# Performance work log

Hardware: AMD Instinct MI355X
Metric: run time of the kernel (lower is better)

Reference implementation:

```python
import jax, jax.numpy as jnp
import numpy as np

# dims (see shape_source)
B, N, P, H, M, E, HOPS = 512, 102, 12, 256, 4, 3, 2
C_CLIP = 10.0   # logit clipping constant params['C']
T = 1.0         # temperature params['T']
NEG = -1e9


def setup_inputs() -> dict:
    key = jax.random.key(0)
    ks = jax.random.split(key, 18)
    s = 0.08  # uniform init range as in _initialize_weights, use scaled normals
    inp = {
        "node_features": jax.random.normal(ks[0], (B, N, P), jnp.float32),
        "adjacency": jax.random.uniform(ks[1], (B, E, N, N), jnp.float32),  # per-edge-cat weighted adjacency
        "mask": jax.random.randint(ks[2], (B, N), 0, 2).astype(jnp.int32),  # 1 = already scheduled / forbidden
        # encoder params
        "W_emb": jax.random.normal(ks[3], (P, H), jnp.float32) * s,
        "W_rel": jax.random.normal(ks[4], (HOPS, E, H, H), jnp.float32) * s / np.sqrt(H),
        "W_self": jax.random.normal(ks[5], (HOPS, H, H), jnp.float32) * s / np.sqrt(H),
        # multi-head glimpse params (Vec / W_q / W_ref per head)
        "Vec": jax.random.normal(ks[6], (M, H, H), jnp.float32) * s,
        "W_q": jax.random.normal(ks[7], (M, 3 * H, H), jnp.float32) * s,
        "W_ref": jax.random.normal(ks[8], (M, H, H), jnp.float32) * s,
        "W_mh": jax.random.normal(ks[9], (M * H, H), jnp.float32) * s,  # multi_head_embedding
        # final pointer params
        "Vec2": jax.random.normal(ks[10], (H,), jnp.float32) * s,
        "W_q2": jax.random.normal(ks[11], (H, H), jnp.float32) * s,
        "W_ref2": jax.random.normal(ks[12], (H, H), jnp.float32) * s,
        # learned decoder seed vectors
        "dec_input": jax.random.normal(ks[13], (H,), jnp.float32) * s,
        "v_1": jax.random.normal(ks[14], (H,), jnp.float32) * s,
    }
    return inp


def reference(node_features, adjacency, mask, W_emb, W_rel, W_self, Vec, W_q,
              W_ref, W_mh, Vec2, W_q2, W_ref2, dec_input, v_1):
    # ---- encoder: linear embedding + HOPS of relational (per-edge-category) message passing ----
    h = jnp.einsum('bnp,ph->bnh', node_features, W_emb)            # [B,N,H]
    for hop in range(HOPS):
        msg = jnp.einsum('benm,bmh->benh', adjacency, h)           # gather neighbors per edge cat
        h = jax.nn.relu(jnp.einsum('benh,ehk->bnk', msg, W_rel[hop])
                        + jnp.einsum('bnh,hk->bnk', h, W_self[hop]))
    enc = h                                                         # [B,N,H]

    # ---- decoder query: cat(graph readout, learned dec_input, learned v_1) -> 3H ----
    enc_mean = enc.mean(axis=1)                                     # [B,H]
    q_cat = jnp.concatenate([enc_mean,
                             jnp.broadcast_to(dec_input, (B, H)),
                             jnp.broadcast_to(v_1, (B, H))], axis=-1)  # [B,3H]

    # ---- multi-head additive (Bahdanau) glimpse: per-head Vec/W_q/W_ref tanh scoring ----
    q = jnp.einsum('bf,mfh->bmh', q_cat, W_q)                       # [B,M,H]
    r = jnp.einsum('bnh,mhk->bmnk', enc, W_ref)                     # [B,M,N,H]
    u = jnp.einsum('bmnh,mhk->bmnk', jnp.tanh(q[:, :, None, :] + r), Vec)
    scores = u.sum(axis=-1)                                         # [B,M,N]
    scores = jnp.where(mask[:, None, :] > 0, NEG, scores)
    a = jax.nn.softmax(scores, axis=-1)
    ctx = jnp.einsum('bmn,bnh->bmh', a, enc).reshape(B, M * H)
    query2 = ctx @ W_mh                                             # [B,H]

    # ---- final pointer head (Vec2 / W_q2 / W_ref2) ----
    u2 = jnp.einsum('h,bnh->bn', Vec2,
                    jnp.tanh((query2 @ W_q2)[:, None, :] + jnp.einsum('bnh,hk->bnk', enc, W_ref2)))
    u2 = C_CLIP * jnp.tanh(u2)                                      # logit clipping
    u2 = jnp.where(mask > 0, NEG, u2)
    log_p = jax.nn.log_softmax(u2 / T, axis=-1)                     # [B,N]
    return log_p
```

## Files before the change

### kernel.cpp

```cpp
#include <hip/hip_runtime.h>
#include <hip/hip_bf16.h>

#define B 512
#define N 102
#define Pdim 12
#define H 256
#define M 4
#define E 3
#define NEG (-1e9f)
#define RT 52224
#define NN 10404

typedef __hip_bfloat16 bf16;
typedef __attribute__((ext_vector_type(8))) short short8;
typedef __attribute__((ext_vector_type(4))) float f32x4;
typedef __attribute__((ext_vector_type(16))) float f32x16;

__device__ __forceinline__ float b2f(bf16 v) { return __bfloat162float(v); }
__device__ __forceinline__ bf16 f2b(float v) { return __float2bfloat16(v); }
__device__ __forceinline__ short f2bs(float v) {
    bf16 t = __float2bfloat16(v);
    return *reinterpret_cast<short*>(&t);
}
__device__ __forceinline__ float fast_tanh(float x) {
    float e = __expf(2.f * x);
    return 1.f - 2.f * __builtin_amdgcn_rcpf(e + 1.f);
}

__global__ __launch_bounds__(256) void wt_prep(const float* __restrict__ Wrel,
                                               const float* __restrict__ Wself,
                                               const float* __restrict__ Wref,
                                               const float* __restrict__ Wref2,
                                               const float* __restrict__ Wmh,
                                               const float* __restrict__ Wq2,
                                               const float* __restrict__ W_q,
                                               const float* __restrict__ Vec,
                                               const float* __restrict__ W_emb,
                                               const float* __restrict__ dec,
                                               const float* __restrict__ v1,
                                               short* __restrict__ wfrag,
                                               short* __restrict__ wrefT,
                                               short* __restrict__ wref2T,
                                               short* __restrict__ wmh_bf,
                                               short* __restrict__ wq2_bf,
                                               short* __restrict__ wq_bf,
                                               short* __restrict__ wembf,
                                               float* __restrict__ qconst,
                                               float* __restrict__ vsum) {
    int bid = blockIdx.x;
    int tid = threadIdx.x;
    __shared__ short tl[1024 * 17];
    if (bid < 32) {
        int hop = bid >> 4, ct = bid & 15;
        for (int i = tid; i < 16384; i += 256) {
            int k = i >> 4, c0 = i & 15;
            int c = ct * 16 + c0;
            float v;
            if (k < 768) v = Wrel[(((size_t)hop * E + (k >> 8)) * H + (k & 255)) * H + c];
            else         v = Wself[((size_t)hop * H + (k - 768)) * H + c];
            tl[k * 17 + c0] = f2bs(v);
        }
        __syncthreads();
        short8* outp = (short8*)wfrag + (size_t)(hop * 16 + ct) * 2048;
        for (int i = tid; i < 2048; i += 256) {
            int ks = i >> 6, lq = i & 63;
            int c0 = lq & 15, kb = (lq >> 4) * 8;
            short8 v;
#pragma unroll
            for (int j = 0; j < 8; ++j) v[j] = tl[(ks * 32 + kb + j) * 17 + c0];
            outp[i] = v;
        }
        return;
    }
    if (bid >= 3648) {
        int m = bid - 3648, hh = tid;
        __shared__ float dls[H], vls[H];
        dls[hh] = dec[hh];
        vls[hh] = v1[hh];
        __syncthreads();
        const float* Wm = W_q + (size_t)m * (3 * H) * H;
        float s = 0.f;
        for (int f = 0; f < H; ++f)
            s += dls[f] * Wm[(H + f) * H + hh] + vls[f] * Wm[(2 * H + f) * H + hh];
        qconst[m * H + hh] = s;
        float vs = 0.f;
        const float* Vr = Vec + ((size_t)m * H + hh) * H;
        for (int k = 0; k < H; ++k) vs += Vr[k];
        vsum[m * H + hh] = vs;
        return;
    }
    int idx = 524288 + (bid - 32) * 256 + tid;
    if (idx < 786432) {
        int r = idx - 524288;
        int row = r >> 8, k = r & 255;
        int m = row >> 8, c = row & 255;
        wrefT[r] = f2bs(Wref[((size_t)m * H + k) * H + c]);
    } else if (idx < 851968) {
        int r = idx - 786432;
        int c = r >> 8, k = r & 255;
        wref2T[r] = f2bs(Wref2[k * H + c]);
    } else if (idx < 1114112) {
        int r = idx - 851968;
        wmh_bf[r] = f2bs(Wmh[r]);
    } else if (idx < 1179648) {
        int r = idx - 1114112;
        wq2_bf[r] = f2bs(Wq2[r]);
    } else if (idx < 1441792) {
        int r = idx - 1179648;
        int m = r >> 16, fh = r & 65535;
        wq_bf[r] = f2bs(W_q[(size_t)m * 768 * 256 + fh]);
    } else if (idx < 1449984) {
        int r = idx - 1441792;
        int ct = r >> 9, lq = (r >> 3) & 63, j = r & 7;
        int c = ct * 16 + (lq & 15), k = (lq >> 4) * 8 + j;
        wembf[r] = (k < Pdim) ? f2bs(W_emb[k * H + c]) : (short)0;
    }
}

#define HP 264
#define YTP 136
#define ASP 136
#define AITER 21
__global__ __launch_bounds__(512, 2) void hop_fused(const bf16* __restrict__ hin,
                                                    const float* __restrict__ nf,
                                                    const short* __restrict__ wembf,
                                                    const float* __restrict__ adj,
                                                    const short* __restrict__ wfragp,
                                                    bf16* __restrict__ hout,
                                                    float* __restrict__ mean_out) {
    int b = blockIdx.x;
    int tid = threadIdx.x;
    int w = tid >> 6;
    int l = tid & 63;
    int cg = l & 15;
    int rg = l >> 4;
    int ct0 = 2 * w, ct1 = 2 * w + 1;

    __shared__ short hS[112 * HP];
    __shared__ short YtS[8 * 32 * YTP];
    __shared__ short AsS[112 * ASP];

    const short8 z8 = {0, 0, 0, 0, 0, 0, 0, 0};
    for (int i = tid; i < (8 * 32 * YTP) / 8; i += 512) ((short8*)YtS)[i] = z8;
    for (int i = tid; i < 10 * 32; i += 512) {
        int n = 102 + (i >> 5), g = i & 31;
        *(short8*)(&hS[n * HP + g * 8]) = z8;
    }
    for (int i = tid; i < 112 * 26; i += 512) {
        int n = i / 26, m = 102 + (i % 26);
        AsS[n * ASP + m] = 0;
    }
    for (int i = tid; i < 10 * 102; i += 512) {
        int n = 102 + i / 102, m = i % 102;
        AsS[n * ASP + m] = 0;
    }
    int offA[AITER];
    {
        const float* Ab0 = adj + (size_t)b * E * NN;
#pragma unroll
        for (int i = 0; i < AITER; ++i) {
            int id = tid + (i << 9);
            if (id < NN) {
                int n = id / N, m = id - n * N;
                offA[i] = n * ASP + m;
                AsS[offA[i]] = f2bs(Ab0[id]);
            } else offA[i] = -1;
        }
    }
    float areg[AITER];
    {
        const float* Ab1 = adj + ((size_t)b * E + 1) * NN;
#pragma unroll
        for (int i = 0; i < AITER; ++i) {
            int id = tid + (i << 9);
            areg[i] = (id < NN) ? Ab1[id] : 0.f;
        }
    }
    if (hin) {
        const short* hp = (const short*)hin;
        for (int i = tid; i < 102 * 32; i += 512) {
            int n = i >> 5, g = i & 31;
            *(short8*)(&hS[n * HP + g * 8]) = *(const short8*)(hp + ((size_t)b * N + n) * H + g * 8);
        }
    } else {
        const short8* we8 = (const short8*)wembf;
        short8 bf0 = we8[ct0 * 64 + l];
        short8 bf1 = we8[ct1 * 64 + l];
#pragma unroll
        for (int nt = 0; nt < 7; ++nt) {
            int row = nt * 16 + cg;
            short8 afr = z8;
            if (row < 102 && rg < 2) {
                const float* src = nf + ((size_t)b * N + row) * Pdim + rg * 8;
                f32x4 v0 = *(const f32x4*)src;
                afr[0] = f2bs(v0[0]); afr[1] = f2bs(v0[1]);
                afr[2] = f2bs(v0[2]); afr[3] = f2bs(v0[3]);
                if (rg == 0) {
                    f32x4 v1 = *(const f32x4*)(src + 4);
                    afr[4] = f2bs(v1[0]); afr[5] = f2bs(v1[1]);
                    afr[6] = f2bs(v1[2]); afr[7] = f2bs(v1[3]);
                }
            }
            f32x4 d0 = (f32x4){0.f, 0.f, 0.f, 0.f}, d1 = d0;
            d0 = __builtin_amdgcn_mfma_f32_16x16x32_bf16(afr, bf0, d0, 0, 0, 0);
            d1 = __builtin_amdgcn_mfma_f32_16x16x32_bf16(afr, bf1, d1, 0, 0, 0);
#pragma unroll
            for (int r = 0; r < 4; ++r) {
                int n = nt * 16 + rg * 4 + r;
                hS[n * HP + ct0 * 16 + cg] = f2bs(d0[r]);
                hS[n * HP + ct1 * 16 + cg] = f2bs(d1[r]);
            }
        }
    }
    __syncthreads();

    const short8* wf8 = (const short8*)wfragp;
    f32x4 hacc0[7], hacc1[7];
#pragma unroll
    for (int j = 0; j < 7; ++j) {
        hacc0[j] = (f32x4){0.f, 0.f, 0.f, 0.f};
        hacc1[j] = hacc0[j];
    }

#pragma unroll
    for (int ks = 0; ks < 8; ++ks) {
        short8 wfs0 = wf8[(ct0 * 32 + 24 + ks) * 64 + l];
        short8 wfs1 = wf8[(ct1 * 32 + 24 + ks) * 64 + l];
#pragma unroll
        for (int nt = 0; nt < 7; ++nt) {
            short8 hf = *(const short8*)(&hS[(nt * 16 + cg) * HP + ks * 32 + rg * 8]);
            hacc0[nt] = __builtin_amdgcn_mfma_f32_16x16x32_bf16(hf, wfs0, hacc0[nt], 0, 0, 0);
            hacc1[nt] = __builtin_amdgcn_mfma_f32_16x16x32_bf16(hf, wfs1, hacc1[nt], 0, 0, 0);
        }
    }

    int ytbase = w * (32 * YTP);
    for (int e = 0; e < E; ++e) {
        if (e > 0) {
            __syncthreads();
#pragma unroll
            for (int i = 0; i < AITER; ++i)
                if (offA[i] >= 0) AsS[offA[i]] = f2bs(areg[i]);
            if (e < E - 1) {
                const float* Abn = adj + ((size_t)b * E + e + 1) * NN;
#pragma unroll
                for (int i = 0; i < AITER; ++i) {
                    int id = tid + (i << 9);
                    if (id < NN) areg[i] = Abn[id];
                }
            }
            __syncthreads();
        }
        f32x4 g0[7], g1[7];
#pragma unroll
        for (int j = 0; j < 7; ++j) {
            g0[j] = (f32x4){0.f, 0.f, 0.f, 0.f};
            g1[j] = g0[j];
        }
#pragma unroll
        for (int ks = 0; ks < 8; ++ks) {
            short8 wfa0 = wf8[(ct0 * 32 + e * 8 + ks) * 64 + l];
            short8 wfa1 = wf8[(ct1 * 32 + e * 8 + ks) * 64 + l];
#pragma unroll
            for (int mt = 0; mt < 7; ++mt) {
                short8 hf = *(const short8*)(&hS[(mt * 16 + cg) * HP + ks * 32 + rg * 8]);
                g0[mt] = __builtin_amdgcn_mfma_f32_16x16x32_bf16(wfa0, hf, g0[mt], 0, 0, 0);
                g1[mt] = __builtin_amdgcn_mfma_f32_16x16x32_bf16(wfa1, hf, g1[mt], 0, 0, 0);
            }
        }
#pragma unroll
        for (int mt = 0; mt < 7; ++mt) {
            int gl = mt * 2 + (cg >> 3);
            int gp0 = ((gl + rg) & 15) * 8 + (cg & 7);
            int gp1 = ((gl + 4 + rg) & 15) * 8 + (cg & 7);
#pragma unroll
            for (int r = 0; r < 4; ++r) {
                YtS[ytbase + (rg * 4 + r) * YTP + gp0] = f2bs(g0[mt][r]);
                YtS[ytbase + (16 + rg * 4 + r) * YTP + gp1] = f2bs(g1[mt][r]);
            }
        }
#pragma unroll
        for (int ks = 0; ks < 4; ++ks) {
            short8 yf0 = *(const short8*)(&YtS[ytbase + cg * YTP +
                                               (((ks * 4 + rg) + (cg >> 2)) & 15) * 8]);
            short8 yf1 = *(const short8*)(&YtS[ytbase + (16 + cg) * YTP +
                                               (((ks * 4 + rg) + 4 + (cg >> 2)) & 15) * 8]);
#pragma unroll
            for (int nt = 0; nt < 7; ++nt) {
                short8 af = *(const short8*)(&AsS[(nt * 16 + cg) * ASP + ks * 32 + rg * 8]);
                hacc0[nt] = __builtin_amdgcn_mfma_f32_16x16x32_bf16(af, yf0, hacc0[nt], 0, 0, 0);
                hacc1[nt] = __builtin_amdgcn_mfma_f32_16x16x32_bf16(af, yf1, hacc1[nt], 0, 0, 0);
            }
        }
    }
    __syncthreads();
#pragma unroll
    for (int nt = 0; nt < 7; ++nt)
#pragma unroll
        for (int r = 0; r < 4; ++r) {
            int n = nt * 16 + rg * 4 + r;
            float v0 = hacc0[nt][r], v1 = hacc1[nt][r];
            hS[n * HP + ct0 * 16 + cg] = f2bs(v0 > 0.f ? v0 : 0.f);
            hS[n * HP + ct1 * 16 + cg] = f2bs(v1 > 0.f ? v1 : 0.f);
        }
    __syncthreads();
    short* ho = (short*)hout;
    for (int i = tid; i < 102 * 32; i += 512) {
        int n = i >> 5, g = i & 31;
        *(short8*)(ho + ((size_t)b * N + n) * H + g * 8) = *(const short8*)(&hS[n * HP + g * 8]);
    }
    if (mean_out) {
        float* partf = (float*)AsS;
        int c = tid & 255, qq = tid >> 8;
        float s = 0.f;
        for (int n = qq; n < N; n += 2) s += b2f(*(const bf16*)&hS[n * HP + c]);
        partf[qq * 256 + c] = s;
        __syncthreads();
        if (tid < 256)
            mean_out[(size_t)b * H + tid] =
                (partf[tid] + partf[256 + tid]) * (1.f / (float)N);
    }
}

__global__ __launch_bounds__(256, 2) void head2_mfma(const bf16* __restrict__ X,
                                                     const short* __restrict__ WT,
                                                     const float* __restrict__ qb, int qbs,
                                                     const float* __restrict__ vsb,
                                                     float* __restrict__ outp, int obs) {
    int rt = blockIdx.x, m = blockIdx.y;
    int r0 = rt * 128;
    int tid = threadIdx.x;
    int w = tid >> 6, l = tid & 63;
    int lr = l & 31;
    int lh = l >> 5;
    __shared__ short Xs[128 * 256];
    __shared__ float qls[3 * 256];
    __shared__ float part[4][128];

    const short* Xp = (const short*)X;
#pragma unroll
    for (int i = 0; i < 16; ++i) {
        int id = tid + i * 256;
        int r = id >> 5, g = id & 31;
        short8 v = *(const short8*)(Xp + (size_t)(r0 + r) * H + g * 8);
        *(short8*)((char*)Xs + r * 512 + ((g ^ (r & 7)) * 16)) = v;
    }
    int b_base = r0 / N;
#pragma unroll
    for (int i = 0; i < 3; ++i) {
        int bb = b_base + i;
        if (bb > B - 1) bb = B - 1;
        qls[i * 256 + tid] = qb[(size_t)bb * qbs + m * H + tid];
    }
    const short8* w8 = (const short8*)WT;
    int cbase = m * 256 + w * 64;
    short8 afr0[16], afr1[16];
#pragma unroll
    for (int ks = 0; ks < 16; ++ks) {
        afr0[ks] = w8[(size_t)(cbase + lr) * 32 + ks * 2 + lh];
        afr1[ks] = w8[(size_t)(cbase + 32 + lr) * 32 + ks * 2 + lh];
    }
    float vsl[32];
#pragma unroll
    for (int j = 0; j < 16; ++j) {
        int cl = (j & 3) + 8 * (j >> 2) + 4 * lh;
        vsl[j]      = vsb[m * H + w * 64 + cl];
        vsl[16 + j] = vsb[m * H + w * 64 + 32 + cl];
    }
    __syncthreads();

    int swz = lr & 7;
    for (int t = 0; t < 4; ++t) {
        f32x16 acc0, acc1;
#pragma unroll
        for (int j = 0; j < 16; ++j) { acc0[j] = 0.f; acc1[j] = 0.f; }
        const char* xbase = (const char*)Xs + (t * 32 + lr) * 512;
#pragma unroll
        for (int ks = 0; ks < 16; ++ks) {
            short8 bx = *(const short8*)(xbase + (((2 * ks + lh) ^ swz) * 16));
            acc0 = __builtin_amdgcn_mfma_f32_32x32x16_bf16(afr0[ks], bx, acc0, 0, 0, 0);
            acc1 = __builtin_amdgcn_mfma_f32_32x32x16_bf16(afr1[ks], bx, acc1, 0, 0, 0);
        }
        int r = r0 + t * 32 + lr;
        int b = r / N;
        int boff = b - b_base;
        float s = 0.f;
#pragma unroll
        for (int j = 0; j < 16; ++j) {
            int cl = (j & 3) + 8 * (j >> 2) + 4 * lh;
            float x0 = qls[boff * 256 + w * 64 + cl] + acc0[j];
            s += fast_tanh(x0) * vsl[j];
            float x1 = qls[boff * 256 + w * 64 + 32 + cl] + acc1[j];
            s += fast_tanh(x1) * vsl[16 + j];
        }
        s += __shfl_xor(s, 32, 64);
        if (l < 32) part[w][t * 32 + lr] = s;
    }
    __syncthreads();
    if (tid < 128) {
        int r = r0 + tid;
        int b = r / N, n = r - b * N;
        outp[(size_t)b * obs + m * N + n] = part[0][tid] + part[1][tid] + part[2][tid] + part[3][tid];
    }
}

__global__ __launch_bounds__(256) void q_k(const float* __restrict__ enc_mean,
                                           const short* __restrict__ wq_bf,
                                           const float* __restrict__ qconst,
                                           float* __restrict__ qbuf) {
    int bid = blockIdx.x;
    int b = bid >> 2, m = bid & 3;
    int hh = threadIdx.x;
    __shared__ float em[H];
    em[hh] = enc_mean[(size_t)b * H + hh];
    __syncthreads();
    const bf16* Wm = (const bf16*)(wq_bf + (size_t)m * 65536);
    float s = qconst[m * H + hh];
    for (int f = 0; f < H; ++f) s += em[f] * b2f(Wm[f * H + hh]);
    qbuf[((size_t)b * M + m) * H + hh] = s;
}

__global__ __launch_bounds__(256) void softmax_ctx_k(const float* __restrict__ scores,
                                                     const int* __restrict__ mask,
                                                     const bf16* __restrict__ enc,
                                                     float* __restrict__ ctx) {
    int bid = blockIdx.x;
    int b = bid >> 2, m = bid & 3;
    int tid = threadIdx.x;
    __shared__ float a[128];
    __shared__ float red[2];
    float sv = NEG;
    if (tid < N)
        sv = (mask[(size_t)b * N + tid] > 0) ? NEG : scores[((size_t)b * M + m) * N + tid];
    if (tid < 128) a[tid] = sv;
    __syncthreads();
    if (tid < 64) {
        float v = fmaxf(a[tid], a[tid + 64]);
        v = fmaxf(v, __shfl_xor(v, 32, 64));
        v = fmaxf(v, __shfl_xor(v, 16, 64));
        v = fmaxf(v, __shfl_xor(v, 8, 64));
        v = fmaxf(v, __shfl_xor(v, 4, 64));
        v = fmaxf(v, __shfl_xor(v, 2, 64));
        v = fmaxf(v, __shfl_xor(v, 1, 64));
        if (tid == 0) red[0] = v;
    }
    __syncthreads();
    float mx = red[0];
    float ev = (tid < N) ? __expf(sv - mx) : 0.f;
    if (tid < 128) a[tid] = ev;
    __syncthreads();
    if (tid < 64) {
        float v = a[tid] + a[tid + 64];
        v += __shfl_xor(v, 32, 64);
        v += __shfl_xor(v, 16, 64);
        v += __shfl_xor(v, 8, 64);
        v += __shfl_xor(v, 4, 64);
        v += __shfl_xor(v, 2, 64);
        v += __shfl_xor(v, 1, 64);
        if (tid == 0) red[1] = __builtin_amdgcn_rcpf(v);
    }
    __syncthreads();
    float inv = red[1];
    float c = 0.f;
    for (int n = 0; n < N; ++n)
        c += a[n] * b2f(enc[((size_t)b * N + n) * H + tid]);
    ctx[((size_t)b * M + m) * H + tid] = c * inv;
}

__global__ __launch_bounds__(256) void query2_k(const float* __restrict__ ctx,
                                                const short* __restrict__ wmh,
                                                const short* __restrict__ wq2,
                                                float* __restrict__ q2) {
    int b = blockIdx.x;
    int tid = threadIdx.x;
    __shared__ float cx[M * H];
    __shared__ float qy[H];
    for (int idx = tid; idx < M * H; idx += 256) cx[idx] = ctx[(size_t)b * M * H + idx];
    __syncthreads();
    const bf16* wm = (const bf16*)wmh;
    float acc = 0.f;
    for (int j = 0; j < M * H; ++j) acc += cx[j] * b2f(wm[(size_t)j * H + tid]);
    qy[tid] = acc;
    __syncthreads();
    const bf16* w2 = (const bf16*)wq2;
    float acc2 = 0.f;
    for (int k = 0; k < H; ++k) acc2 += qy[k] * b2f(w2[(size_t)k * H + tid]);
    q2[(size_t)b * H + tid] = acc2;
}

__global__ __launch_bounds__(128) void final_out_k(const float* __restrict__ u2,
                                                   const int* __restrict__ mask,
                                                   float* __restrict__ out) {
    int b = blockIdx.x;
    int tid = threadIdx.x;
    __shared__ float a[128];
    __shared__ float red[2];
    float u = NEG;
    if (tid < N) {
        u = 10.f * fast_tanh(u2[(size_t)b * N + tid]);
        if (mask[(size_t)b * N + tid] > 0) u = NEG;
    }
    a[tid] = u;
    __syncthreads();
    if (tid < 64) {
        float v = fmaxf(a[tid], a[tid + 64]);
        v = fmaxf(v, __shfl_xor(v, 32, 64));
        v = fmaxf(v, __shfl_xor(v, 16, 64));
        v = fmaxf(v, __shfl_xor(v, 8, 64));
        v = fmaxf(v, __shfl_xor(v, 4, 64));
        v = fmaxf(v, __shfl_xor(v, 2, 64));
        v = fmaxf(v, __shfl_xor(v, 1, 64));
        if (tid == 0) red[0] = v;
    }
    __syncthreads();
    float mx = red[0];
    float ev = (tid < N) ? __expf(u - mx) : 0.f;
    a[tid] = ev;
    __syncthreads();
    if (tid < 64) {
        float v = a[tid] + a[tid + 64];
        v += __shfl_xor(v, 32, 64);
        v += __shfl_xor(v, 16, 64);
        v += __shfl_xor(v, 8, 64);
        v += __shfl_xor(v, 4, 64);
        v += __shfl_xor(v, 2, 64);
        v += __shfl_xor(v, 1, 64);
        if (tid == 0) red[1] = logf(v);
    }
    __syncthreads();
    if (tid < N) out[(size_t)b * N + tid] = (u - mx) - red[1];
}

extern "C" void kernel_launch(void* const* d_in, const int* in_sizes, int n_in,
                              void* d_out, int out_size, void* d_ws, size_t ws_size,
                              hipStream_t stream) {
    const float* nf     = (const float*)d_in[0];
    const float* adj    = (const float*)d_in[1];
    const int*   mask   = (const int*)d_in[2];
    const float* W_emb  = (const float*)d_in[3];
    const float* W_rel  = (const float*)d_in[4];
    const float* W_self = (const float*)d_in[5];
    const float* Vec    = (const float*)d_in[6];
    const float* W_q    = (const float*)d_in[7];
    const float* W_ref  = (const float*)d_in[8];
    const float* W_mh   = (const float*)d_in[9];
    const float* Vec2   = (const float*)d_in[10];
    const float* W_q2   = (const float*)d_in[11];
    const float* W_ref2 = (const float*)d_in[12];
    const float* dec    = (const float*)d_in[13];
    const float* v_1    = (const float*)d_in[14];
    float* out = (float*)d_out;

    char* p = (char*)d_ws;
    size_t off = 0;
    auto alloc = [&](size_t bytes) -> char* {
        char* q = p + off;
        off += (bytes + 255) & ~(size_t)255;
        return q;
    };
    bf16* hA    = (bf16*)alloc((size_t)RT * H * sizeof(bf16));
    bf16* hB    = (bf16*)alloc((size_t)RT * H * sizeof(bf16));
    short* wfrag  = (short*)alloc(524288 * sizeof(short));
    short* wrefT  = (short*)alloc(262144 * sizeof(short));
    short* wref2T = (short*)alloc(65536 * sizeof(short));
    short* wmh_bf = (short*)alloc(262144 * sizeof(short));
    short* wq2_bf = (short*)alloc(65536 * sizeof(short));
    short* wq_bf  = (short*)alloc(262144 * sizeof(short));
    short* wembf  = (short*)alloc(8192 * sizeof(short));
    float* enc_mean = (float*)alloc((size_t)B * H * sizeof(float));
    float* qconst   = (float*)alloc((size_t)M * H * sizeof(float));
    float* vsumb    = (float*)alloc((size_t)M * H * sizeof(float));
    float* qbuf     = (float*)alloc((size_t)B * M * H * sizeof(float));
    float* scoresb  = (float*)alloc((size_t)B * M * N * sizeof(float));
    float* ctxb     = (float*)alloc((size_t)B * M * H * sizeof(float));
    float* q2b      = (float*)alloc((size_t)B * H * sizeof(float));
    float* u2b      = (float*)alloc((size_t)B * N * sizeof(float));

    wt_prep<<<3652, 256, 0, stream>>>(W_rel, W_self, W_ref, W_ref2, W_mh, W_q2,
                                      W_q, Vec, W_emb, dec, v_1,
                                      wfrag, wrefT, wref2T, wmh_bf, wq2_bf, wq_bf, wembf,
                                      qconst, vsumb);

    hop_fused<<<B, 512, 0, stream>>>(nullptr, nf, wembf, adj, wfrag, hB, nullptr);
    hop_fused<<<B, 512, 0, stream>>>(hB, nullptr, wembf, adj, wfrag + 262144, hA, enc_mean);

    const bf16* enc = hA;

    q_k<<<B * M, 256, 0, stream>>>(enc_mean, wq_bf, qconst, qbuf);
    head2_mfma<<<dim3(RT / 128, M), 256, 0, stream>>>(enc, wrefT, qbuf, M * H, vsumb, scoresb, M * N);
    softmax_ctx_k<<<B * M, 256, 0, stream>>>(scoresb, mask, enc, ctxb);
    query2_k<<<B, 256, 0, stream>>>(ctxb, wmh_bf, wq2_bf, q2b);
    head2_mfma<<<dim3(RT / 128, 1), 256, 0, stream>>>(enc, wref2T, q2b, H, Vec2, u2b, N);
    final_out_k<<<B, 128, 0, stream>>>(u2b, mask, out);
}
```

Measured before the change: 331.4 us.

## Fuse both encoder hops into one kernel with pre-padded bf16 adjacency

```diff
diff --git a/kernel.cpp b/kernel.cpp
--- a/kernel.cpp
+++ b/kernel.cpp
@@ -38,6 +38,7 @@
                                                const float* __restrict__ W_emb,
                                                const float* __restrict__ dec,
                                                const float* __restrict__ v1,
+                                               const float* __restrict__ adj,
                                                short* __restrict__ wfrag,
                                                short* __restrict__ wrefT,
                                                short* __restrict__ wref2T,
@@ -45,11 +46,24 @@
                                                short* __restrict__ wq2_bf,
                                                short* __restrict__ wq_bf,
                                                short* __restrict__ wembf,
+                                               short* __restrict__ adjp,
                                                float* __restrict__ qconst,
                                                float* __restrict__ vsum) {
     int bid = blockIdx.x;
     int tid = threadIdx.x;
     __shared__ short tl[1024 * 17];
+    if (bid >= 3652) {
+        int be = bid - 3652;
+        const float* src = adj + (size_t)be * NN;
+        short* dst = adjp + (size_t)be * (112 * 128);
+        for (int i = tid; i < 112 * 128; i += 256) {
+            int n = i >> 7, m = i & 127;
+            short v = 0;
+            if (n < N && m < N) v = f2bs(src[n * N + m]);
+            dst[i] = v;
+        }
+        return;
+    }
     if (bid < 32) {
         int hop = bid >> 4, ct = bid & 15;
         for (int i = tid; i < 16384; i += 256) {
@@ -118,15 +132,13 @@
 }
 
 #define HP 264
-#define YTP 136
+#define YP2 136
 #define ASP 136
-#define AITER 21
-__global__ __launch_bounds__(512, 2) void hop_fused(const bf16* __restrict__ hin,
-                                                    const float* __restrict__ nf,
+__global__ __launch_bounds__(512, 2) void enc_fused(const float* __restrict__ nf,
                                                     const short* __restrict__ wembf,
-                                                    const float* __restrict__ adj,
+                                                    const short* __restrict__ adjp,
                                                     const short* __restrict__ wfragp,
-                                                    bf16* __restrict__ hout,
+                                                    bf16* __restrict__ enc_out,
                                                     float* __restrict__ mean_out) {
     int b = blockIdx.x;
     int tid = threadIdx.x;
@@ -134,58 +146,26 @@
     int l = tid & 63;
     int cg = l & 15;
     int rg = l >> 4;
-    int ct0 = 2 * w, ct1 = 2 * w + 1;
+    int ct0 = 2 * w, ct1 = ct0 + 1;
 
     __shared__ short hS[112 * HP];
-    __shared__ short YtS[8 * 32 * YTP];
+    __shared__ short YtS[256 * YP2];
     __shared__ short AsS[112 * ASP];
 
     const short8 z8 = {0, 0, 0, 0, 0, 0, 0, 0};
-    for (int i = tid; i < (8 * 32 * YTP) / 8; i += 512) ((short8*)YtS)[i] = z8;
     for (int i = tid; i < 10 * 32; i += 512) {
         int n = 102 + (i >> 5), g = i & 31;
         *(short8*)(&hS[n * HP + g * 8]) = z8;
     }
-    for (int i = tid; i < 112 * 26; i += 512) {
-        int n = i / 26, m = 102 + (i % 26);
-        AsS[n * ASP + m] = 0;
-    }
-    for (int i = tid; i < 10 * 102; i += 512) {
-        int n = 102 + i / 102, m = i % 102;
-        AsS[n * ASP + m] = 0;
-    }
-    int offA[AITER];
     {
-        const float* Ab0 = adj + (size_t)b * E * NN;
-#pragma unroll
-        for (int i = 0; i < AITER; ++i) {
-            int id = tid + (i << 9);
-            if (id < NN) {
-                int n = id / N, m = id - n * N;
-                offA[i] = n * ASP + m;
-                AsS[offA[i]] = f2bs(Ab0[id]);
-            } else offA[i] = -1;
-        }
-    }
-    float areg[AITER];
+        int c = tid >> 1, g = 14 + (tid & 1);
+        *(short8*)(&YtS[c * YP2 + g * 8]) = z8;
+    }
+
     {
-        const float* Ab1 = adj + ((size_t)b * E + 1) * NN;
-#pragma unroll
-        for (int i = 0; i < AITER; ++i) {
-            int id = tid + (i << 9);
-            areg[i] = (id < NN) ? Ab1[id] : 0.f;
-        }
-    }
-    if (hin) {
-        const short* hp = (const short*)hin;
-        for (int i = tid; i < 102 * 32; i += 512) {
-            int n = i >> 5, g = i & 31;
-            *(short8*)(&hS[n * HP + g * 8]) = *(const short8*)(hp + ((size_t)b * N + n) * H + g * 8);
-        }
-    } else {
         const short8* we8 = (const short8*)wembf;
-        short8 bf0 = we8[ct0 * 64 + l];
-        short8 bf1 = we8[ct1 * 64 + l];
+        short8 bfe0 = we8[ct0 * 64 + l];
+        short8 bfe1 = we8[ct1 * 64 + l];
 #pragma unroll
         for (int nt = 0; nt < 7; ++nt) {
             int row = nt * 16 + cg;
@@ -202,8 +182,8 @@
                 }
             }
             f32x4 d0 = (f32x4){0.f, 0.f, 0.f, 0.f}, d1 = d0;
-            d0 = __builtin_amdgcn_mfma_f32_16x16x32_bf16(afr, bf0, d0, 0, 0, 0);
-            d1 = __builtin_amdgcn_mfma_f32_16x16x32_bf16(afr, bf1, d1, 0, 0, 0);
+            d0 = __builtin_amdgcn_mfma_f32_16x16x32_bf16(afr, bfe0, d0, 0, 0, 0);
+            d1 = __builtin_amdgcn_mfma_f32_16x16x32_bf16(afr, bfe1, d1, 0, 0, 0);
 #pragma unroll
             for (int r = 0; r < 4; ++r) {
                 int n = nt * 16 + rg * 4 + r;
@@ -214,102 +194,92 @@
     }
     __syncthreads();
 
-    const short8* wf8 = (const short8*)wfragp;
-    f32x4 hacc0[7], hacc1[7];
-#pragma unroll
-    for (int j = 0; j < 7; ++j) {
-        hacc0[j] = (f32x4){0.f, 0.f, 0.f, 0.f};
-        hacc1[j] = hacc0[j];
-    }
-
-#pragma unroll
-    for (int ks = 0; ks < 8; ++ks) {
-        short8 wfs0 = wf8[(ct0 * 32 + 24 + ks) * 64 + l];
-        short8 wfs1 = wf8[(ct1 * 32 + 24 + ks) * 64 + l];
-#pragma unroll
-        for (int nt = 0; nt < 7; ++nt) {
-            short8 hf = *(const short8*)(&hS[(nt * 16 + cg) * HP + ks * 32 + rg * 8]);
-            hacc0[nt] = __builtin_amdgcn_mfma_f32_16x16x32_bf16(hf, wfs0, hacc0[nt], 0, 0, 0);
-            hacc1[nt] = __builtin_amdgcn_mfma_f32_16x16x32_bf16(hf, wfs1, hacc1[nt], 0, 0, 0);
-        }
-    }
-
-    int ytbase = w * (32 * YTP);
-    for (int e = 0; e < E; ++e) {
-        if (e > 0) {
+    for (int hop = 0; hop < 2; ++hop) {
+        const short8* wf8 = ((const short8*)wfragp) + (size_t)hop * 32768;
+        f32x4 hacc0[7], hacc1[7];
+#pragma unroll
+        for (int j = 0; j < 7; ++j) {
+            hacc0[j] = (f32x4){0.f, 0.f, 0.f, 0.f};
+            hacc1[j] = hacc0[j];
+        }
+
+        for (int e = 0; e < E; ++e) {
+            const short8* Ap = (const short8*)adjp + (size_t)(b * E + e) * 1792;
+            for (int i = tid; i < 1792; i += 512) {
+                int n = i >> 4, g = i & 15;
+                *(short8*)(&AsS[n * ASP + g * 8]) = Ap[i];
+            }
+            if (e == 0) {
+#pragma unroll
+                for (int ks = 0; ks < 8; ++ks) {
+                    short8 wfs0 = wf8[(ct0 * 32 + 24 + ks) * 64 + l];
+                    short8 wfs1 = wf8[(ct1 * 32 + 24 + ks) * 64 + l];
+#pragma unroll
+                    for (int nt = 0; nt < 7; ++nt) {
+                        short8 hf = *(const short8*)(&hS[(nt * 16 + cg) * HP + ks * 32 + rg * 8]);
+                        hacc0[nt] = __builtin_amdgcn_mfma_f32_16x16x32_bf16(hf, wfs0, hacc0[nt], 0, 0, 0);
+                        hacc1[nt] = __builtin_amdgcn_mfma_f32_16x16x32_bf16(hf, wfs1, hacc1[nt], 0, 0, 0);
+                    }
+                }
+            }
+            f32x4 g0[7], g1[7];
+#pragma unroll
+            for (int j = 0; j < 7; ++j) {
+                g0[j] = (f32x4){0.f, 0.f, 0.f, 0.f};
+                g1[j] = g0[j];
+            }
+#pragma unroll
+            for (int ks = 0; ks < 8; ++ks) {
+                short8 wfa0 = wf8[(ct0 * 32 + e * 8 + ks) * 64 + l];
+                short8 wfa1 = wf8[(ct1 * 32 + e * 8 + ks) * 64 + l];
+#pragma unroll
+                for (int mt = 0; mt < 7; ++mt) {
+                    short8 hf = *(const short8*)(&hS[(mt * 16 + cg) * HP + ks * 32 + rg * 8]);
+                    g0[mt] = __builtin_amdgcn_mfma_f32_16x16x32_bf16(wfa0, hf, g0[mt], 0, 0, 0);
+                    g1[mt] = __builtin_amdgcn_mfma_f32_16x16x32_bf16(wfa1, hf, g1[mt], 0, 0, 0);
+                }
+            }
+#pragma unroll
+            for (int mt = 0; mt < 7; ++mt)
+#pragma unroll
+                for (int r = 0; r < 4; ++r) {
+                    int c0 = ct0 * 16 + rg * 4 + r;
+                    int c1 = ct1 * 16 + rg * 4 + r;
+                    YtS[c0 * YP2 + mt * 16 + cg] = f2bs(g0[mt][r]);
+                    YtS[c1 * YP2 + mt * 16 + cg] = f2bs(g1[mt][r]);
+                }
             __syncthreads();
 #pragma unroll
-            for (int i = 0; i < AITER; ++i)
-                if (offA[i] >= 0) AsS[offA[i]] = f2bs(areg[i]);
-            if (e < E - 1) {
-                const float* Abn = adj + ((size_t)b * E + e + 1) * NN;
-#pragma unroll
-                for (int i = 0; i < AITER; ++i) {
-                    int id = tid + (i << 9);
-                    if (id < NN) areg[i] = Abn[id];
+            for (int ks = 0; ks < 4; ++ks) {
+                short8 yf0 = *(const short8*)(&YtS[(ct0 * 16 + cg) * YP2 + (ks * 4 + rg) * 8]);
+                short8 yf1 = *(const short8*)(&YtS[(ct1 * 16 + cg) * YP2 + (ks * 4 + rg) * 8]);
+#pragma unroll
+                for (int nt = 0; nt < 7; ++nt) {
+                    short8 af = *(const short8*)(&AsS[(nt * 16 + cg) * ASP + ks * 32 + rg * 8]);
+                    hacc0[nt] = __builtin_amdgcn_mfma_f32_16x16x32_bf16(af, yf0, hacc0[nt], 0, 0, 0);
+                    hacc1[nt] = __builtin_amdgcn_mfma_f32_16x16x32_bf16(af, yf1, hacc1[nt], 0, 0, 0);
                 }
             }
             __syncthreads();
         }
-        f32x4 g0[7], g1[7];
-#pragma unroll
-        for (int j = 0; j < 7; ++j) {
-            g0[j] = (f32x4){0.f, 0.f, 0.f, 0.f};
-            g1[j] = g0[j];
-        }
-#pragma unroll
-        for (int ks = 0; ks < 8; ++ks) {
-            short8 wfa0 = wf8[(ct0 * 32 + e * 8 + ks) * 64 + l];
-            short8 wfa1 = wf8[(ct1 * 32 + e * 8 + ks) * 64 + l];
-#pragma unroll
-            for (int mt = 0; mt < 7; ++mt) {
-                short8 hf = *(const short8*)(&hS[(mt * 16 + cg) * HP + ks * 32 + rg * 8]);
-                g0[mt] = __builtin_amdgcn_mfma_f32_16x16x32_bf16(wfa0, hf, g0[mt], 0, 0, 0);
-                g1[mt] = __builtin_amdgcn_mfma_f32_16x16x32_bf16(wfa1, hf, g1[mt], 0, 0, 0);
-            }
-        }
-#pragma unroll
-        for (int mt = 0; mt < 7; ++mt) {
-            int gl = mt * 2 + (cg >> 3);
-            int gp0 = ((gl + rg) & 15) * 8 + (cg & 7);
-            int gp1 = ((gl + 4 + rg) & 15) * 8 + (cg & 7);
+#pragma unroll
+        for (int nt = 0; nt < 7; ++nt)
 #pragma unroll
             for (int r = 0; r < 4; ++r) {
-                YtS[ytbase + (rg * 4 + r) * YTP + gp0] = f2bs(g0[mt][r]);
-                YtS[ytbase + (16 + rg * 4 + r) * YTP + gp1] = f2bs(g1[mt][r]);
-            }
-        }
-#pragma unroll
-        for (int ks = 0; ks < 4; ++ks) {
-            short8 yf0 = *(const short8*)(&YtS[ytbase + cg * YTP +
-                                               (((ks * 4 + rg) + (cg >> 2)) & 15) * 8]);
-            short8 yf1 = *(const short8*)(&YtS[ytbase + (16 + cg) * YTP +
-                                               (((ks * 4 + rg) + 4 + (cg >> 2)) & 15) * 8]);
-#pragma unroll
-            for (int nt = 0; nt < 7; ++nt) {
-                short8 af = *(const short8*)(&AsS[(nt * 16 + cg) * ASP + ks * 32 + rg * 8]);
-                hacc0[nt] = __builtin_amdgcn_mfma_f32_16x16x32_bf16(af, yf0, hacc0[nt], 0, 0, 0);
-                hacc1[nt] = __builtin_amdgcn_mfma_f32_16x16x32_bf16(af, yf1, hacc1[nt], 0, 0, 0);
-            }
-        }
-    }
-    __syncthreads();
-#pragma unroll
-    for (int nt = 0; nt < 7; ++nt)
-#pragma unroll
-        for (int r = 0; r < 4; ++r) {
-            int n = nt * 16 + rg * 4 + r;
-            float v0 = hacc0[nt][r], v1 = hacc1[nt][r];
-            hS[n * HP + ct0 * 16 + cg] = f2bs(v0 > 0.f ? v0 : 0.f);
-            hS[n * HP + ct1 * 16 + cg] = f2bs(v1 > 0.f ? v1 : 0.f);
-        }
-    __syncthreads();
-    short* ho = (short*)hout;
+                int n = nt * 16 + rg * 4 + r;
+                float v0 = hacc0[nt][r], v1 = hacc1[nt][r];
+                hS[n * HP + ct0 * 16 + cg] = f2bs(v0 > 0.f ? v0 : 0.f);
+                hS[n * HP + ct1 * 16 + cg] = f2bs(v1 > 0.f ? v1 : 0.f);
+            }
+        __syncthreads();
+    }
+
+    short* ho = (short*)enc_out;
     for (int i = tid; i < 102 * 32; i += 512) {
         int n = i >> 5, g = i & 31;
         *(short8*)(ho + ((size_t)b * N + n) * H + g * 8) = *(const short8*)(&hS[n * HP + g * 8]);
     }
-    if (mean_out) {
+    {
         float* partf = (float*)AsS;
         int c = tid & 255, qq = tid >> 8;
         float s = 0.f;
@@ -317,8 +287,7 @@
         partf[qq * 256 + c] = s;
         __syncthreads();
         if (tid < 256)
-            mean_out[(size_t)b * H + tid] =
-                (partf[tid] + partf[256 + tid]) * (1.f / (float)N);
+            mean_out[(size_t)b * H + tid] = (partf[tid] + partf[256 + tid]) * (1.f / (float)N);
     }
 }
 
@@ -558,8 +527,8 @@
         off += (bytes + 255) & ~(size_t)255;
         return q;
     };
-    bf16* hA    = (bf16*)alloc((size_t)RT * H * sizeof(bf16));
-    bf16* hB    = (bf16*)alloc((size_t)RT * H * sizeof(bf16));
+    bf16* hA      = (bf16*)alloc((size_t)RT * H * sizeof(bf16));
+    short* adjp   = (short*)alloc((size_t)B * E * 112 * 128 * sizeof(short));
     short* wfrag  = (short*)alloc(524288 * sizeof(short));
     short* wrefT  = (short*)alloc(262144 * sizeof(short));
     short* wref2T = (short*)alloc(65536 * sizeof(short));
@@ -576,13 +545,12 @@
     float* q2b      = (float*)alloc((size_t)B * H * sizeof(float));
     float* u2b      = (float*)alloc((size_t)B * N * sizeof(float));
 
-    wt_prep<<<3652, 256, 0, stream>>>(W_rel, W_self, W_ref, W_ref2, W_mh, W_q2,
-                                      W_q, Vec, W_emb, dec, v_1,
+    wt_prep<<<5188, 256, 0, stream>>>(W_rel, W_self, W_ref, W_ref2, W_mh, W_q2,
+                                      W_q, Vec, W_emb, dec, v_1, adj,
                                       wfrag, wrefT, wref2T, wmh_bf, wq2_bf, wq_bf, wembf,
-                                      qconst, vsumb);
-
-    hop_fused<<<B, 512, 0, stream>>>(nullptr, nf, wembf, adj, wfrag, hB, nullptr);
-    hop_fused<<<B, 512, 0, stream>>>(hB, nullptr, wembf, adj, wfrag + 262144, hA, enc_mean);
+                                      adjp, qconst, vsumb);
+
+    enc_fused<<<B, 512, 0, stream>>>(nf, wembf, adjp, wfrag, hA, enc_mean);
 
     const bf16* enc = hA;
 
```

Measured after the change: 270.1 us. 18.5% less time.
